# Optimization experiments

Hardware: AMD Instinct MI355X
Metric: run time of the kernel (lower is better)

Reference implementation:

```python
import jax, jax.numpy as jnp
import numpy as np

B, T, D = 2, 2048, 1024
N_HEADS, D_HEAD, WINDOW = 16, 64, 256
SCALE = D_HEAD ** -0.5


def setup_inputs() -> dict:
    key = jax.random.key(0)
    k1, k2, k3 = jax.random.split(key, 3)
    x = jax.random.normal(k1, (B, T, D), dtype=jnp.float32)
    # torch Linear weights are [out_features, in_features], init std=0.02
    w_qkv = jax.random.normal(k2, (3 * N_HEADS * D_HEAD, D), dtype=jnp.float32) * 0.02
    w_out = jax.random.normal(k3, (D, N_HEADS * D_HEAD), dtype=jnp.float32) * 0.02
    return {"x": x, "w_qkv": w_qkv, "w_out": w_out}


def reference(x, w_qkv, w_out):
    b, t, d = x.shape
    qkv = jnp.einsum('btd,ed->bte', x, w_qkv)  # [B,T,3*H*Dh]
    q, k, v = jnp.split(qkv, 3, axis=-1)
    def heads(u):
        return u.reshape(b, t, N_HEADS, D_HEAD).transpose(0, 2, 1, 3)  # [B,H,T,Dh]
    q, k, v = heads(q), heads(k), heads(v)
    scores = jnp.einsum('bhqd,bhkd->bhqk', q, k) * SCALE  # [B,H,T,T]
    pos = jnp.arange(t)
    dist = pos[:, None] - pos[None, :]  # query - key
    allowed = (dist >= 0) & (dist < WINDOW)  # causal sliding window
    neg_inf = jnp.asarray(-jnp.inf, dtype=scores.dtype)
    scores = jnp.where(allowed[None, None], scores, neg_inf)
    attn = jax.nn.softmax(scores, axis=-1)
    out = jnp.einsum('bhqk,bhkd->bhqd', attn, v)  # [B,H,T,Dh]
    out = out.transpose(0, 2, 1, 3).reshape(b, t, N_HEADS * D_HEAD)
    return jnp.einsum('bte,de->btd', out, w_out)
```

## Files before the change

kernel.cpp:

```cpp
#include <hip/hip_runtime.h>
#include <hip/hip_bf16.h>

typedef unsigned short bfu;
typedef __attribute__((ext_vector_type(8))) short short8;
typedef __attribute__((ext_vector_type(4))) float floatx4;
typedef __attribute__((ext_vector_type(2))) __fp16 fp16x2;
typedef __attribute__((ext_vector_type(4))) _Float16 half4v;

#define B_ 2
#define T_ 2048
#define D_ 1024
#define NH 16
#define DH 64
#define WIN 256
#define QKV_COLS 3072
#define NX  (B_ * T_ * D_)
#define NWQ (QKV_COLS * D_)
#define NWO (D_ * D_)

__device__ __forceinline__ bfu f2b_bits(float f) {
  union { __hip_bfloat16 h; bfu u; } cv;
  cv.h = __float2bfloat16(f);
  return cv.u;
}

__device__ __forceinline__ void gl_lds16(const bfu* g, bfu* l) {
  __builtin_amdgcn_global_load_lds(
      (const __attribute__((address_space(1))) unsigned int*)g,
      (__attribute__((address_space(3))) unsigned int*)l, 16, 0, 0);
}

#define BARRIER() __builtin_amdgcn_s_barrier()

__global__ void cvt3_kernel(const float* __restrict__ x, const float* __restrict__ wq,
                            const float* __restrict__ wo, bfu* __restrict__ out) {
  int i = (blockIdx.x * 256 + threadIdx.x) * 4;
  const float* src;
  int off;
  if (i < NX)            { src = x;  off = 0; }
  else if (i < NX + NWQ) { src = wq; off = NX; }
  else                   { src = wo; off = NX + NWQ; }
  floatx4 v = *(const floatx4*)(src + (i - off));
  out[i + 0] = f2b_bits(v.x);
  out[i + 1] = f2b_bits(v.y);
  out[i + 2] = f2b_bits(v.z);
  out[i + 3] = f2b_bits(v.w);
}

template <int EPI, int TN>
__global__ __launch_bounds__(256) void gemm_bt_kernel(const bfu* __restrict__ A,
                                                      const bfu* __restrict__ Bm,
                                                      void* __restrict__ C,
                                                      int M, int N, int K) {
  constexpr int NJ = TN / 32;
  __shared__ __align__(16) bfu As[128][64];
  __shared__ __align__(16) bfu Bs[TN][64];
  const int tid = threadIdx.x;
  const int wave = tid >> 6, lane = tid & 63;
  const int quad = lane >> 4, cl = lane & 15;
  const int lr = lane >> 3, lg = lane & 7, sg = lg ^ lr;
  const int wm = (wave >> 1) * 64, wn = (wave & 1) * (TN / 2);
  const int m0 = blockIdx.y * 128, n0 = blockIdx.x * TN;

  floatx4 acc[4][NJ] = {};

  for (int k0 = 0; k0 < K; k0 += 64) {
    __syncthreads();
#pragma unroll
    for (int i = 0; i < 4; ++i) {
      const int row = i * 32 + wave * 8;
      gl_lds16(A + (size_t)(m0 + row + lr) * K + k0 + sg * 8, &As[row][0]);
    }
#pragma unroll
    for (int i = 0; i < TN / 32; ++i) {
      const int row = i * 32 + wave * 8;
      gl_lds16(Bm + (size_t)(n0 + row + lr) * K + k0 + sg * 8, &Bs[row][0]);
    }
    __syncthreads();
#pragma unroll
    for (int ks = 0; ks < 2; ++ks) {
      const int gsw = ks * 4 + quad;
      short8 af[4], bfr[NJ];
#pragma unroll
      for (int im = 0; im < 4; ++im)
        af[im] = *(const short8*)(&As[wm + im * 16 + cl][(gsw ^ (cl & 7)) << 3]);
#pragma unroll
      for (int in = 0; in < NJ; ++in)
        bfr[in] = *(const short8*)(&Bs[wn + in * 16 + cl][(gsw ^ (cl & 7)) << 3]);
#pragma unroll
      for (int im = 0; im < 4; ++im)
#pragma unroll
        for (int in = 0; in < NJ; ++in)
          acc[im][in] = __builtin_amdgcn_mfma_f32_16x16x32_bf16(af[im], bfr[in], acc[im][in], 0, 0, 0);
    }
  }
  const float qs = (EPI == 2 && n0 < 1024) ? 0.125f : 1.0f;
  const bool vf16 = (EPI == 2) && (n0 >= 2048);
#pragma unroll
  for (int im = 0; im < 4; ++im) {
#pragma unroll
    for (int r = 0; r < 4; ++r) {
      const size_t row = (size_t)(m0 + wm + im * 16 + quad * 4 + r);
#pragma unroll
      for (int in = 0; in < NJ; ++in) {
        const size_t idx = row * (size_t)N + (n0 + wn + in * 16 + cl);
        const float val = acc[im][in][r];
        if constexpr (EPI == 0) {
          ((float*)C)[idx] = val;
        } else {
          bfu bits;
          if (vf16) { union { _Float16 h; bfu u; } cv; cv.h = (_Float16)val; bits = cv.u; }
          else      { bits = f2b_bits(val * qs); }
          ((bfu*)C)[idx] = bits;
        }
      }
    }
  }
}

__global__ __launch_bounds__(512, 2) void gemm8p_qkv_kernel(const bfu* __restrict__ A,
                                                            const bfu* __restrict__ Bm,
                                                            bfu* __restrict__ C,
                                                            int M, int N, int K) {
  __shared__ __align__(16) bfu As[2][256][64];
  __shared__ __align__(16) bfu Bs[2][256][64];
  const int tid = threadIdx.x;
  const int wave = tid >> 6, lane = tid & 63;
  const int quad = lane >> 4, cl = lane & 15;
  const int lr = lane >> 3, lg = lane & 7, sg = lg ^ lr;

  const int cpx = gridDim.x >> 3;
  const int swz = (blockIdx.x & 7) * cpx + (blockIdx.x >> 3);
  const int ntile = N >> 8;
  const int m0 = (swz / ntile) * 256, n0 = (swz % ntile) * 256;
  const int wmRow = (wave >> 2) * 128;
  const int wnCol = (wave & 3) * 64;

  floatx4 acc[8][4] = {};
  const int NT = K >> 6;

  auto stageA = [&](int buf, int r0, int k0s) {
    gl_lds16(A + (size_t)(m0 + r0 + lr) * K + k0s + sg * 8, &As[buf][r0][0]);
  };
  auto stageB = [&](int buf, int r0, int k0s) {
    gl_lds16(Bm + (size_t)(n0 + r0 + lr) * K + k0s + sg * 8, &Bs[buf][r0][0]);
  };
  const int a0 = wave * 8;
  const int b0 = (wave >> 2) * 64 + (wave & 3) * 8;

  auto ldA = [&](int buf, int rbase, int ks) -> short8 {
    return *(const short8*)(&As[buf][rbase + cl][((ks * 4 + quad) ^ (cl & 7)) << 3]);
  };
  auto ldB = [&](int buf, int rbase, int ks) -> short8 {
    return *(const short8*)(&Bs[buf][rbase + cl][((ks * 4 + quad) ^ (cl & 7)) << 3]);
  };

  stageA(0, a0, 0);          stageA(0, 128 + a0, 0);
  stageB(0, b0, 0);          stageB(0, 128 + b0, 0);
  stageB(0, b0 + 32, 0);     stageB(0, 128 + b0 + 32, 0);
  stageA(0, 64 + a0, 0);     stageA(0, 192 + a0, 0);
  asm volatile("s_waitcnt vmcnt(4)");
  BARRIER();

  for (int t = 0; t < NT; ++t) {
    const int cur = t & 1, nxt = cur ^ 1;
    const int kn = (t + 1) << 6;
    const bool pf = (t + 1 < NT);
    short8 af[4][2], bf0[2][2], bf1[2][2];

#pragma unroll
    for (int ks = 0; ks < 2; ++ks) {
#pragma unroll
      for (int im = 0; im < 4; ++im) af[im][ks] = ldA(cur, wmRow + im * 16, ks);
#pragma unroll
      for (int in = 0; in < 2; ++in) bf0[in][ks] = ldB(cur, wnCol + in * 16, ks);
    }
    if (pf) {
      stageA(nxt, a0, kn);      stageA(nxt, 128 + a0, kn);
      stageB(nxt, b0, kn);      stageB(nxt, 128 + b0, kn);
      asm volatile("s_waitcnt vmcnt(6)");
    } else {
      asm volatile("s_waitcnt vmcnt(2)");
    }
    BARRIER();
    __builtin_amdgcn_s_setprio(1);
#pragma unroll
    for (int ks = 0; ks < 2; ++ks)
#pragma unroll
      for (int im = 0; im < 4; ++im)
#pragma unroll
        for (int in = 0; in < 2; ++in)
          acc[im][in] = __builtin_amdgcn_mfma_f32_16x16x32_bf16(af[im][ks], bf0[in][ks], acc[im][in], 0, 0, 0);
    __builtin_amdgcn_s_setprio(0);
    BARRIER();

#pragma unroll
    for (int ks = 0; ks < 2; ++ks)
#pragma unroll
      for (int in = 0; in < 2; ++in) bf1[in][ks] = ldB(cur, wnCol + 32 + in * 16, ks);
    if (pf) {
      stageB(nxt, b0 + 32, kn); stageB(nxt, 128 + b0 + 32, kn);
      asm volatile("s_waitcnt vmcnt(6)");
    } else {
      asm volatile("s_waitcnt vmcnt(0)");
    }
    BARRIER();
    __builtin_amdgcn_s_setprio(1);
#pragma unroll
    for (int ks = 0; ks < 2; ++ks)
#pragma unroll
      for (int im = 0; im < 4; ++im)
#pragma unroll
        for (int in = 0; in < 2; ++in)
          acc[im][2 + in] = __builtin_amdgcn_mfma_f32_16x16x32_bf16(af[im][ks], bf1[in][ks], acc[im][2 + in], 0, 0, 0);
    __builtin_amdgcn_s_setprio(0);
    BARRIER();

#pragma unroll
    for (int ks = 0; ks < 2; ++ks)
#pragma unroll
      for (int im = 0; im < 4; ++im) af[im][ks] = ldA(cur, wmRow + 64 + im * 16, ks);
    if (pf) {
      stageA(nxt, 64 + a0, kn); stageA(nxt, 192 + a0, kn);
    }
    BARRIER();
    __builtin_amdgcn_s_setprio(1);
#pragma unroll
    for (int ks = 0; ks < 2; ++ks)
#pragma unroll
      for (int im = 0; im < 4; ++im)
#pragma unroll
        for (int in = 0; in < 2; ++in)
          acc[4 + im][2 + in] = __builtin_amdgcn_mfma_f32_16x16x32_bf16(af[im][ks], bf1[in][ks], acc[4 + im][2 + in], 0, 0, 0);
    __builtin_amdgcn_s_setprio(0);
    BARRIER();

    if (pf) asm volatile("s_waitcnt vmcnt(4)");
    BARRIER();
    __builtin_amdgcn_s_setprio(1);
#pragma unroll
    for (int ks = 0; ks < 2; ++ks)
#pragma unroll
      for (int im = 0; im < 4; ++im)
#pragma unroll
        for (int in = 0; in < 2; ++in)
          acc[4 + im][in] = __builtin_amdgcn_mfma_f32_16x16x32_bf16(af[im][ks], bf0[in][ks], acc[4 + im][in], 0, 0, 0);
    __builtin_amdgcn_s_setprio(0);
    BARRIER();
  }

  const float qs = (n0 < 1024) ? 0.125f : 1.0f;
  const bool vf16 = (n0 >= 2048);
#pragma unroll
  for (int qm = 0; qm < 2; ++qm) {
#pragma unroll
    for (int im = 0; im < 4; ++im) {
#pragma unroll
      for (int r = 0; r < 4; ++r) {
        const size_t row = (size_t)(m0 + wmRow + qm * 64 + im * 16 + quad * 4 + r);
#pragma unroll
        for (int qn = 0; qn < 2; ++qn) {
#pragma unroll
          for (int in = 0; in < 2; ++in) {
            const size_t idx = row * (size_t)N + (n0 + wnCol + qn * 32 + in * 16 + cl);
            const float val = acc[qm * 4 + im][qn * 2 + in][r];
            bfu bits;
            if (vf16) { union { _Float16 h; bfu u; } cv; cv.h = (_Float16)val; bits = cv.u; }
            else      { bits = f2b_bits(val * qs); }
            C[idx] = bits;
          }
        }
      }
    }
  }
}

__global__ __launch_bounds__(512, 4) void swa_kernel(const bfu* __restrict__ qkv,
                                                     bfu* __restrict__ aout) {
  __shared__ __align__(16) bfu Qs[128][64];
  __shared__ __align__(16) bfu Ks[2][64][64];
  __shared__ __align__(16) bfu Vs[2][64][64];

  const int qt = blockIdx.x, h = blockIdx.y, b = blockIdx.z;
  const int tid = threadIdx.x, wave = tid >> 6, lane = tid & 63;
  const int quad = lane >> 4, cl = lane & 15;
  const int lr = lane >> 3, lg = lane & 7, sg = lg ^ lr;
  const int q0 = qt * 128;
  const bfu* qb = qkv + (size_t)b * T_ * QKV_COLS + h * DH;
  const bfu* kb = qb + 1024;
  const bfu* vb = qb + 2048;

  const int jt0 = (qt >= 2) ? 2 * qt - 4 : 0;
  const int njt = (2 * qt + 1) - jt0 + 1;

  const int vrow = tid >> 3;
  const int vcol = (tid & 7) * 8;

#pragma unroll
  for (int i = 0; i < 2; ++i) {
    const int row = wave * 16 + i * 8;
    gl_lds16(qb + (size_t)(q0 + row + lr) * QKV_COLS + sg * 8, &Qs[row][0]);
  }
  gl_lds16(kb + (size_t)(jt0 * 64 + wave * 8 + lr) * QKV_COLS + sg * 8, &Ks[0][wave * 8][0]);
  {
    union { short8 v; bfu u[8]; } t0;
    t0.v = *(const short8*)(vb + (size_t)(jt0 * 64 + vrow) * QKV_COLS + vcol);
#pragma unroll
    for (int e = 0; e < 8; ++e) {
      const int d = vcol + e;
      const int gp = ((vrow >> 2) + d + (d >> 3)) & 15;
      Vs[0][d][gp * 4 + (vrow & 3)] = t0.u[e];
    }
  }
  __syncthreads();

  float l_acc = 0.f;
  floatx4 acc[4] = {};
  const int ddc = cl + (cl >> 3);
  const int qw0 = q0 + wave * 16;

  for (int it = 0; it < njt; ++it) {
    const int cur = it & 1, nxt = cur ^ 1;
    const int k0 = (jt0 + it) * 64;
    const bool pf = (it + 1 < njt);

    union { short8 v; bfu u[8]; } vp;
    if (pf) {
      const int kn = k0 + 64;
      gl_lds16(kb + (size_t)(kn + wave * 8 + lr) * QKV_COLS + sg * 8, &Ks[nxt][wave * 8][0]);
      vp.v = *(const short8*)(vb + (size_t)(kn + vrow) * QKV_COLS + vcol);
    }

    bool live[4];
#pragma unroll
    for (int jk = 0; jk < 4; ++jk) {
      const int kg0 = k0 + jk * 16;
      live[jk] = (qw0 + 15 >= kg0) && (qw0 <= kg0 + 270);
    }

    floatx4 s[4] = {};
#pragma unroll
    for (int ks = 0; ks < 2; ++ks) {
      const int col = ((ks * 4 + quad) ^ (cl & 7)) << 3;
      short8 bq = *(const short8*)(&Qs[wave * 16 + cl][col]);
#pragma unroll
      for (int jk = 0; jk < 4; ++jk)
        if (live[jk]) {
          short8 ak = *(const short8*)(&Ks[cur][jk * 16 + cl][col]);
          s[jk] = __builtin_amdgcn_mfma_f32_16x16x32_bf16(ak, bq, s[jk], 0, 0, 0);
        }
    }

    const int qg = qw0 + cl;
    half4v af[4] = {};
#pragma unroll
    for (int jk = 0; jk < 4; ++jk) {
      if (!live[jk]) continue;
      float p[4];
#pragma unroll
      for (int r = 0; r < 4; ++r) {
        const int kg = k0 + jk * 16 + quad * 4 + r;
        const int dist = qg - kg;
        p[r] = (dist >= 0 && dist < WIN) ? __expf(s[jk][r]) : 0.f;
        l_acc += p[r];
      }
      union { fp16x2 h2[2]; half4v h4; } u;
      u.h2[0] = __builtin_amdgcn_cvt_pkrtz(p[0], p[1]);
      u.h2[1] = __builtin_amdgcn_cvt_pkrtz(p[2], p[3]);
      af[jk] = u.h4;
    }

#pragma unroll
    for (int kt = 0; kt < 4; ++kt) {
      if (!live[kt]) continue;
#pragma unroll
      for (int jd = 0; jd < 4; ++jd) {
        const int d = jd * 16 + cl;
        const int gp = (kt * 4 + quad + ddc + jd * 2) & 15;
        half4v bv = *(const half4v*)(&Vs[cur][d][gp * 4]);
        acc[jd] = __builtin_amdgcn_mfma_f32_16x16x16f16(af[kt], bv, acc[jd], 0, 0, 0);
      }
    }

    if (pf) {
#pragma unroll
      for (int e = 0; e < 8; ++e) {
        const int d = vcol + e;
        const int gp = ((vrow >> 2) + d + (d >> 3)) & 15;
        Vs[nxt][d][gp * 4 + (vrow & 3)] = vp.u[e];
      }
    }
    __syncthreads();
  }

  l_acc += __shfl_xor(l_acc, 16);
  l_acc += __shfl_xor(l_acc, 32);
  const float linv = 1.f / l_acc;
  float lq[4];
#pragma unroll
  for (int r = 0; r < 4; ++r) lq[r] = __shfl(linv, quad * 4 + r);

  bfu* ob = aout + (size_t)b * T_ * D_ + h * DH;
#pragma unroll
  for (int r = 0; r < 4; ++r) {
    const size_t row = (size_t)(q0 + wave * 16 + quad * 4 + r);
#pragma unroll
    for (int jd = 0; jd < 4; ++jd)
      ob[row * D_ + jd * 16 + cl] = f2b_bits(acc[jd][r] * lq[r]);
  }
}

extern "C" void kernel_launch(void* const* d_in, const int* in_sizes, int n_in,
                              void* d_out, int out_size, void* d_ws, size_t ws_size,
                              hipStream_t stream) {
  const float* x     = (const float*)d_in[0];
  const float* w_qkv = (const float*)d_in[1];
  const float* w_out = (const float*)d_in[2];
  float* out = (float*)d_out;
  char* ws = (char*)d_ws;

  bfu* xb    = (bfu*)(ws);
  bfu* wqkvb = (bfu*)(ws + (8ull << 20));
  bfu* woutb = (bfu*)(ws + (14ull << 20));
  bfu* qkvb  = (bfu*)(ws + (16ull << 20));
  bfu* attb  = (bfu*)(ws + (40ull << 20));

  cvt3_kernel<<<(NX + NWQ + NWO) / 1024, 256, 0, stream>>>(x, w_qkv, w_out, xb);

  gemm8p_qkv_kernel<<<dim3(192), 512, 0, stream>>>(xb, wqkvb, qkvb, B_ * T_, QKV_COLS, D_);

  swa_kernel<<<dim3(T_ / 128, NH, B_), 512, 0, stream>>>(qkvb, attb);

  gemm_bt_kernel<0, 64><<<dim3(D_ / 64, (B_ * T_) / 128), 256, 0, stream>>>(
      attb, woutb, out, B_ * T_, D_, D_);
}
```

Before: 153.5 us.

## Retile QKV GEMM to 256x192 tiles for 256 blocks with fewer barriers

Changes the QKV projection GEMM tile from 256x256 to 256x192 so the grid grows from 192 to 256 blocks, matching the 256 compute units of the device better. Each wave now computes a 128x48 sub-tile with 3 N-fragments, and the main loop is restructured from four MFMA phases to two, removing several barriers and rescheduling the global-to-LDS prefetches and waitcnts. The per-column scaling and fp16/bf16 choice moves into the epilogue per fragment, since a 192-wide tile can straddle the Q/K/V boundaries. The cost is lower arithmetic intensity per block, and the hand-tuned waitcnt counts must stay correct for the new load pattern.

```diff
diff --git a/kernel.cpp b/kernel.cpp
--- a/kernel.cpp
+++ b/kernel.cpp
@@ -123,7 +123,7 @@
                                                             bfu* __restrict__ C,
                                                             int M, int N, int K) {
   __shared__ __align__(16) bfu As[2][256][64];
-  __shared__ __align__(16) bfu Bs[2][256][64];
+  __shared__ __align__(16) bfu Bs[2][192][64];
   const int tid = threadIdx.x;
   const int wave = tid >> 6, lane = tid & 63;
   const int quad = lane >> 4, cl = lane & 15;
@@ -131,12 +131,11 @@
 
   const int cpx = gridDim.x >> 3;
   const int swz = (blockIdx.x & 7) * cpx + (blockIdx.x >> 3);
-  const int ntile = N >> 8;
-  const int m0 = (swz / ntile) * 256, n0 = (swz % ntile) * 256;
+  const int m0 = (swz >> 4) * 256, n0 = (swz & 15) * 192;
   const int wmRow = (wave >> 2) * 128;
-  const int wnCol = (wave & 3) * 64;
-
-  floatx4 acc[8][4] = {};
+  const int wnCol = (wave & 3) * 48;
+
+  floatx4 acc[2][4][3] = {};
   const int NT = K >> 6;
 
   auto stageA = [&](int buf, int r0, int k0s) {
@@ -146,7 +145,7 @@
     gl_lds16(Bm + (size_t)(n0 + r0 + lr) * K + k0s + sg * 8, &Bs[buf][r0][0]);
   };
   const int a0 = wave * 8;
-  const int b0 = (wave >> 2) * 64 + (wave & 3) * 8;
+  const int bc0 = wave * 24;
 
   auto ldA = [&](int buf, int rbase, int ks) -> short8 {
     return *(const short8*)(&As[buf][rbase + cl][((ks * 4 + quad) ^ (cl & 7)) << 3]);
@@ -155,65 +154,40 @@
     return *(const short8*)(&Bs[buf][rbase + cl][((ks * 4 + quad) ^ (cl & 7)) << 3]);
   };
 
-  stageA(0, a0, 0);          stageA(0, 128 + a0, 0);
-  stageB(0, b0, 0);          stageB(0, 128 + b0, 0);
-  stageB(0, b0 + 32, 0);     stageB(0, 128 + b0 + 32, 0);
-  stageA(0, 64 + a0, 0);     stageA(0, 192 + a0, 0);
-  asm volatile("s_waitcnt vmcnt(4)");
+  stageA(0, a0, 0);        stageA(0, 128 + a0, 0);
+  stageB(0, bc0, 0);       stageB(0, bc0 + 8, 0);   stageB(0, bc0 + 16, 0);
+  stageA(0, 64 + a0, 0);   stageA(0, 192 + a0, 0);
+  asm volatile("s_waitcnt vmcnt(2)");
   BARRIER();
 
   for (int t = 0; t < NT; ++t) {
     const int cur = t & 1, nxt = cur ^ 1;
     const int kn = (t + 1) << 6;
     const bool pf = (t + 1 < NT);
-    short8 af[4][2], bf0[2][2], bf1[2][2];
+    short8 af[4][2], bfv[3][2];
 
 #pragma unroll
     for (int ks = 0; ks < 2; ++ks) {
 #pragma unroll
       for (int im = 0; im < 4; ++im) af[im][ks] = ldA(cur, wmRow + im * 16, ks);
 #pragma unroll
-      for (int in = 0; in < 2; ++in) bf0[in][ks] = ldB(cur, wnCol + in * 16, ks);
+      for (int nf = 0; nf < 3; ++nf) bfv[nf][ks] = ldB(cur, wnCol + nf * 16, ks);
     }
     if (pf) {
       stageA(nxt, a0, kn);      stageA(nxt, 128 + a0, kn);
-      stageB(nxt, b0, kn);      stageB(nxt, 128 + b0, kn);
-      asm volatile("s_waitcnt vmcnt(6)");
-    } else {
-      asm volatile("s_waitcnt vmcnt(2)");
-    }
-    BARRIER();
+      stageB(nxt, bc0, kn);     stageB(nxt, bc0 + 8, kn);  stageB(nxt, bc0 + 16, kn);
+    }
     __builtin_amdgcn_s_setprio(1);
 #pragma unroll
     for (int ks = 0; ks < 2; ++ks)
 #pragma unroll
       for (int im = 0; im < 4; ++im)
 #pragma unroll
-        for (int in = 0; in < 2; ++in)
-          acc[im][in] = __builtin_amdgcn_mfma_f32_16x16x32_bf16(af[im][ks], bf0[in][ks], acc[im][in], 0, 0, 0);
+        for (int nf = 0; nf < 3; ++nf)
+          acc[0][im][nf] = __builtin_amdgcn_mfma_f32_16x16x32_bf16(af[im][ks], bfv[nf][ks], acc[0][im][nf], 0, 0, 0);
     __builtin_amdgcn_s_setprio(0);
-    BARRIER();
-
-#pragma unroll
-    for (int ks = 0; ks < 2; ++ks)
-#pragma unroll
-      for (int in = 0; in < 2; ++in) bf1[in][ks] = ldB(cur, wnCol + 32 + in * 16, ks);
-    if (pf) {
-      stageB(nxt, b0 + 32, kn); stageB(nxt, 128 + b0 + 32, kn);
-      asm volatile("s_waitcnt vmcnt(6)");
-    } else {
-      asm volatile("s_waitcnt vmcnt(0)");
-    }
-    BARRIER();
-    __builtin_amdgcn_s_setprio(1);
-#pragma unroll
-    for (int ks = 0; ks < 2; ++ks)
-#pragma unroll
-      for (int im = 0; im < 4; ++im)
-#pragma unroll
-        for (int in = 0; in < 2; ++in)
-          acc[im][2 + in] = __builtin_amdgcn_mfma_f32_16x16x32_bf16(af[im][ks], bf1[in][ks], acc[im][2 + in], 0, 0, 0);
-    __builtin_amdgcn_s_setprio(0);
+    if (pf) asm volatile("s_waitcnt vmcnt(5)");
+    else    asm volatile("s_waitcnt vmcnt(0)");
     BARRIER();
 
 #pragma unroll
@@ -223,34 +197,19 @@
     if (pf) {
       stageA(nxt, 64 + a0, kn); stageA(nxt, 192 + a0, kn);
     }
+    __builtin_amdgcn_s_setprio(1);
+#pragma unroll
+    for (int ks = 0; ks < 2; ++ks)
+#pragma unroll
+      for (int im = 0; im < 4; ++im)
+#pragma unroll
+        for (int nf = 0; nf < 3; ++nf)
+          acc[1][im][nf] = __builtin_amdgcn_mfma_f32_16x16x32_bf16(af[im][ks], bfv[nf][ks], acc[1][im][nf], 0, 0, 0);
+    __builtin_amdgcn_s_setprio(0);
+    if (pf) asm volatile("s_waitcnt vmcnt(2)");
     BARRIER();
-    __builtin_amdgcn_s_setprio(1);
-#pragma unroll
-    for (int ks = 0; ks < 2; ++ks)
-#pragma unroll
-      for (int im = 0; im < 4; ++im)
-#pragma unroll
-        for (int in = 0; in < 2; ++in)
-          acc[4 + im][2 + in] = __builtin_amdgcn_mfma_f32_16x16x32_bf16(af[im][ks], bf1[in][ks], acc[4 + im][2 + in], 0, 0, 0);
-    __builtin_amdgcn_s_setprio(0);
-    BARRIER();
-
-    if (pf) asm volatile("s_waitcnt vmcnt(4)");
-    BARRIER();
-    __builtin_amdgcn_s_setprio(1);
-#pragma unroll
-    for (int ks = 0; ks < 2; ++ks)
-#pragma unroll
-      for (int im = 0; im < 4; ++im)
-#pragma unroll
-        for (int in = 0; in < 2; ++in)
-          acc[4 + im][in] = __builtin_amdgcn_mfma_f32_16x16x32_bf16(af[im][ks], bf0[in][ks], acc[4 + im][in], 0, 0, 0);
-    __builtin_amdgcn_s_setprio(0);
-    BARRIER();
-  }
-
-  const float qs = (n0 < 1024) ? 0.125f : 1.0f;
-  const bool vf16 = (n0 >= 2048);
+  }
+
 #pragma unroll
   for (int qm = 0; qm < 2; ++qm) {
 #pragma unroll
@@ -259,16 +218,16 @@
       for (int r = 0; r < 4; ++r) {
         const size_t row = (size_t)(m0 + wmRow + qm * 64 + im * 16 + quad * 4 + r);
 #pragma unroll
-        for (int qn = 0; qn < 2; ++qn) {
-#pragma unroll
-          for (int in = 0; in < 2; ++in) {
-            const size_t idx = row * (size_t)N + (n0 + wnCol + qn * 32 + in * 16 + cl);
-            const float val = acc[qm * 4 + im][qn * 2 + in][r];
-            bfu bits;
-            if (vf16) { union { _Float16 h; bfu u; } cv; cv.h = (_Float16)val; bits = cv.u; }
-            else      { bits = f2b_bits(val * qs); }
-            C[idx] = bits;
-          }
+        for (int nf = 0; nf < 3; ++nf) {
+          const int colb = n0 + wnCol + nf * 16;
+          const float qs = (colb < 1024) ? 0.125f : 1.0f;
+          const bool vf16 = (colb >= 2048);
+          const size_t idx = row * (size_t)N + colb + cl;
+          const float val = acc[qm][im][nf][r];
+          bfu bits;
+          if (vf16) { union { _Float16 h; bfu u; } cv; cv.h = (_Float16)val; bits = cv.u; }
+          else      { bits = f2b_bits(val * qs); }
+          C[idx] = bits;
         }
       }
     }
@@ -427,7 +386,7 @@
 
   cvt3_kernel<<<(NX + NWQ + NWO) / 1024, 256, 0, stream>>>(x, w_qkv, w_out, xb);
 
-  gemm8p_qkv_kernel<<<dim3(192), 512, 0, stream>>>(xb, wqkvb, qkvb, B_ * T_, QKV_COLS, D_);
+  gemm8p_qkv_kernel<<<dim3(256), 512, 0, stream>>>(xb, wqkvb, qkvb, B_ * T_, QKV_COLS, D_);
 
   swa_kernel<<<dim3(T_ / 128, NH, B_), 512, 0, stream>>>(qkvb, attb);
 
```

Result: faster. 145.3 us (-5.3%).
